# Performance work log

Measured on AMD Instinct MI355X. Metric: run time of the kernel, lower is better.

The kernel has to match this reference:

```python
import jax, jax.numpy as jnp
import numpy as np

D = 256   # input_size
H = 512   # hidden_size
A = 4     # alpha_dim
K = 2 * A * A  # output values per input dim (binary=False -> 2 params)


def _masks():
    # MADE sequential-ordering masks, per DART.create_masks
    in_deg = np.arange(D)
    hid_deg = np.arange(H) % (D - 1)
    out_deg = np.arange(D) - 1  # arange(D) % D - 1
    m0 = (hid_deg[:, None] >= in_deg[None, :]).astype(np.float32)   # [H, D]
    mh = (hid_deg[:, None] >= hid_deg[None, :]).astype(np.float32)  # [H, H]
    ml = (out_deg[:, None] >= hid_deg[None, :]).astype(np.float32)  # [D, H]
    # repeat(1, K).view(-1, H): each output-dim row repeated K consecutive times
    ml = np.repeat(ml, K, axis=0)                                    # [D*K, H]
    return jnp.asarray(m0), jnp.asarray(mh), jnp.asarray(ml)


def setup_inputs() -> dict:
    key = jax.random.key(0)
    ks = jax.random.split(key, 10)
    B = 1024
    x = jax.random.normal(ks[0], (B, D), dtype=jnp.float32)
    def lin(k, out_dim, in_dim):
        s = 1.0 / np.sqrt(in_dim)
        kw, kb = jax.random.split(k)
        W = jax.random.uniform(kw, (out_dim, in_dim), jnp.float32, -s, s)
        b = jax.random.uniform(kb, (out_dim,), jnp.float32, -s, s)
        return W, b
    W0, b0 = lin(ks[1], H, D)
    W1, b1 = lin(ks[2], H, H)
    W2, b2 = lin(ks[3], H, H)
    Wout, bout = lin(ks[4], D * K, H)
    # unnormalized_log_p_alpha initialized to log(1/A)
    ulpa = jnp.full((1, D - 1, 1, A), -np.log(A), dtype=jnp.float32)
    return {"x": x, "W0": W0, "b0": b0, "W1": W1, "b1": b1,
            "W2": W2, "b2": b2, "Wout": Wout, "bout": bout, "ulpa": ulpa}


def reference(x, W0, b0, W1, b1, W2, b2, Wout, bout, ulpa):
    m0, mh, ml = _masks()
    B = x.shape[0]
    # masked MLP (MADE)
    h = jax.nn.relu(x @ (m0 * W0).T + b0)
    h = jax.nn.relu(h @ (mh * W1).T + b1)
    h = jax.nn.relu(h @ (mh * W2).T + b2)
    theta = (h @ (ml * Wout).T + bout).reshape(B, D, 2, A, A)
    mu = theta[:, :, 0]                      # [B, D, A, A]
    std = jnp.exp(theta[:, :, 1]) + 0.01     # [B, D, A, A]
    xe = x[:, :, None, None]
    # Normal log-prob
    log_px = -0.5 * jnp.square((xe - mu) / std) - jnp.log(std) - 0.5 * jnp.log(2.0 * jnp.pi)
    # normalized log p(alpha): [1, D-1, 1, A]
    lpa = jax.nn.log_softmax(ulpa, axis=-1)
    joint = log_px[:, :-1] + lpa             # [B, D-1, A, A]
    first = joint[:, 0, 0:1]                 # [B, 1, A]
    inner = jnp.swapaxes(joint[:, 1:], 0, 1)  # [D-2, B, A, A]
    # HMM-style forward recursion: stable log-domain chain matmul via scan
    def step(carry, m):
        # carry: [B, 1, A]; m: [B, A, A]
        new = jax.nn.logsumexp(carry[:, :, :, None] + m[:, None, :, :], axis=-2)
        return new, None
    carry, _ = jax.lax.scan(step, first, inner)
    last = log_px[:, -1, :, 0:1]             # [B, A, 1]
    log_p = jax.nn.logsumexp(carry[:, :, :, None] + last[:, None, :, :], axis=-2)  # [B,1,1]
    return log_p, theta
```

## Files before the change

### kernel.cpp

```cpp
#include <hip/hip_runtime.h>
#include <math.h>

#define Bsz 1024
#define Dd  256
#define Hh  512
#define NOUT 8192
#define C0f 0.91893853320467274178f

typedef __attribute__((ext_vector_type(8))) short bf8_t;
typedef __attribute__((ext_vector_type(4))) float f4_t;

__device__ inline ushort f2b(float f) {
  union { float f; unsigned u; } c; c.f = f;
  unsigned r = c.u + 0x7fffu + ((c.u >> 16) & 1u);
  return (ushort)(r >> 16);
}

__device__ inline void async16(const void* g, void* l) {
  __builtin_amdgcn_global_load_lds((const __attribute__((address_space(1))) void*)g,
                                   (__attribute__((address_space(3))) void*)l, 16, 0, 0);
}

__device__ inline int mod255(int v) {
  if (v >= 510) return v - 510;
  if (v >= 255) return v - 255;
  return v;
}

__global__ __launch_bounds__(256) void prep(
    const float* __restrict__ x,  const float* __restrict__ W0,
    const float* __restrict__ W1, const float* __restrict__ W2,
    const float* __restrict__ Wout, const float* __restrict__ ulpa,
    ushort* __restrict__ xb, ushort* __restrict__ w0b, ushort* __restrict__ w1b,
    ushort* __restrict__ w2b, ushort* __restrict__ woutb,
    float* __restrict__ lpa)
{
  const int blk = blockIdx.x, tid = threadIdx.x;
  if (blk == 2496) {
    if (tid < Dd - 1) {
      float v0 = ulpa[tid * 4 + 0], v1 = ulpa[tid * 4 + 1];
      float v2 = ulpa[tid * 4 + 2], v3 = ulpa[tid * 4 + 3];
      float m = fmaxf(fmaxf(v0, v1), fmaxf(v2, v3));
      float s = __expf(v0 - m) + __expf(v1 - m) + __expf(v2 - m) + __expf(v3 - m);
      float l = m + __logf(s);
      lpa[tid * 4 + 0] = v0 - l;
      lpa[tid * 4 + 1] = v1 - l;
      lpa[tid * 4 + 2] = v2 - l;
      lpa[tid * 4 + 3] = v3 - l;
    }
    return;
  }
  const float* src; ushort* dst; int lb, mode;
  if (blk < 128)      { src = x;    dst = xb;    lb = blk;       mode = 0; }
  else if (blk < 192) { src = W0;   dst = w0b;   lb = blk - 128; mode = 1; }
  else if (blk < 320) { src = W1;   dst = w1b;   lb = blk - 192; mode = 2; }
  else if (blk < 448) { src = W2;   dst = w2b;   lb = blk - 320; mode = 2; }
  else                { src = Wout; dst = woutb; lb = blk - 448; mode = 3; }

  const int e = lb * 2048 + tid * 8;
  float4 v0 = *(const float4*)(src + e);
  float4 v1 = *(const float4*)(src + e + 4);
  float vv[8] = {v0.x, v0.y, v0.z, v0.w, v1.x, v1.y, v1.z, v1.w};
  ushort u[8];
  if (mode == 0) {
#pragma unroll
    for (int i = 0; i < 8; i++) u[i] = f2b(vv[i]);
  } else if (mode == 1) {
    int n = e >> 8, k0 = e & 255, nd = mod255(n);
#pragma unroll
    for (int i = 0; i < 8; i++) u[i] = (nd >= k0 + i) ? f2b(vv[i]) : (ushort)0;
  } else if (mode == 2) {
    int n = e >> 9, k0 = e & 511, nd = mod255(n);
#pragma unroll
    for (int i = 0; i < 8; i++) u[i] = (nd >= mod255(k0 + i)) ? f2b(vv[i]) : (ushort)0;
  } else {
    int n = e >> 9, k0 = e & 511, nd = (n >> 5) - 1;
#pragma unroll
    for (int i = 0; i < 8; i++) u[i] = (nd >= mod255(k0 + i)) ? f2b(vv[i]) : (ushort)0;
  }
  *(ushort4*)(dst + e)     = *(ushort4*)&u[0];
  *(ushort4*)(dst + e + 4) = *(ushort4*)&u[4];
}

template<int KD>
__global__ __launch_bounds__(256) void gemm_s(
    const ushort* __restrict__ A, const ushort* __restrict__ W,
    const float* __restrict__ bias, ushort* __restrict__ Ch)
{
  __shared__ ushort As[32 * 64];
  __shared__ ushort Bs[32 * 64];
  const int tid = threadIdx.x, lane = tid & 63, wave = tid >> 6;
  const int row0 = blockIdx.y * 32, col0 = blockIdx.x * 32;
  const int wi = wave >> 1, wj = wave & 1;
  const int fm = lane & 15, qq = lane >> 4;
  const int srow = lane >> 3, qslot = lane & 7;

  f4_t acc = (f4_t){0.f, 0.f, 0.f, 0.f};

  for (int kt = 0; kt < KD; kt += 64) {
    {
      int rb = wave * 8;
      int r = rb + srow;
      int q = (qslot - r) & 7;
      async16(A + (size_t)(row0 + r) * KD + kt + q * 8, &As[rb * 64]);
      async16(W + (size_t)(col0 + r) * KD + kt + q * 8, &Bs[rb * 64]);
    }
    __syncthreads();
#pragma unroll
    for (int t = 0; t < 2; t++) {
      int ra = wi * 16 + fm;
      int slota = ((t * 4 + qq) + ra) & 7;
      bf8_t af = *(const bf8_t*)&As[ra * 64 + slota * 8];
      int rb = wj * 16 + fm;
      int slot = ((t * 4 + qq) + rb) & 7;
      bf8_t bf = *(const bf8_t*)&Bs[rb * 64 + slot * 8];
      acc = __builtin_amdgcn_mfma_f32_16x16x32_bf16(af, bf, acc, 0, 0, 0);
    }
    __syncthreads();
  }

  int col = col0 + wj * 16 + fm;
  float bv = bias[col];
  int rbase = row0 + wi * 16 + qq * 4;
#pragma unroll
  for (int r = 0; r < 4; r++) {
    float t = fmaxf(acc[r] + bv, 0.0f);
    Ch[(size_t)(rbase + r) * Hh + col] = f2b(t);
  }
}

__global__ __launch_bounds__(256) void gemm_big(
    const ushort* __restrict__ A, const ushort* __restrict__ W,
    const float* __restrict__ bias, float* __restrict__ Cf)
{
  __shared__ ushort As[128 * 64];
  __shared__ ushort Bs[64 * 64];
  const int tid = threadIdx.x, lane = tid & 63, wave = tid >> 6;
  const int waveM = wave >> 1, waveN = wave & 1;
  const int row0 = blockIdx.y * 128, col0 = blockIdx.x * 64;
  const int dm = 2 * (int)blockIdx.x;
  const int fm = lane & 15, qq = lane >> 4;
  const int srow = lane >> 3, qslot = lane & 7;
  const int Kd = Hh, N = NOUT;

  f4_t acc[4][2];
#pragma unroll
  for (int i = 0; i < 4; i++)
#pragma unroll
    for (int j = 0; j < 2; j++) acc[i][j] = (f4_t){0.f, 0.f, 0.f, 0.f};

  for (int kt = 0; kt < Kd; kt += 64) {
    bool needed = (kt <= dm) || (kt >= 192 && kt <= 255 + dm) || (kt == 448);
    if (!needed) continue;
#pragma unroll
    for (int p = 0; p < 4; p++) {
      int rb = p * 32 + wave * 8;
      int r = rb + srow;
      int q = (qslot - r) & 7;
      async16(A + (size_t)(row0 + r) * Kd + kt + q * 8, &As[rb * 64]);
    }
#pragma unroll
    for (int p = 0; p < 2; p++) {
      int rb = p * 32 + wave * 8;
      int r = rb + srow;
      int q = (qslot - r) & 7;
      async16(W + (size_t)(col0 + r) * Kd + kt + q * 8, &Bs[rb * 64]);
    }
    __syncthreads();
#pragma unroll
    for (int t = 0; t < 2; t++) {
      bf8_t af[4], bf[2];
#pragma unroll
      for (int i = 0; i < 4; i++) {
        int r = waveM * 64 + i * 16 + fm;
        int slot = ((t * 4 + qq) + r) & 7;
        af[i] = *(const bf8_t*)&As[r * 64 + slot * 8];
      }
#pragma unroll
      for (int j = 0; j < 2; j++) {
        int r = waveN * 32 + j * 16 + fm;
        int slot = ((t * 4 + qq) + r) & 7;
        bf[j] = *(const bf8_t*)&Bs[r * 64 + slot * 8];
      }
#pragma unroll
      for (int i = 0; i < 4; i++)
#pragma unroll
        for (int j = 0; j < 2; j++)
          acc[i][j] = __builtin_amdgcn_mfma_f32_16x16x32_bf16(af[i], bf[j], acc[i][j], 0, 0, 0);
    }
    __syncthreads();
  }

#pragma unroll
  for (int j = 0; j < 2; j++) {
    int col = col0 + waveN * 32 + j * 16 + fm;
    float bv = bias[col];
#pragma unroll
    for (int i = 0; i < 4; i++) {
      int rbase = row0 + waveM * 64 + i * 16 + qq * 4;
#pragma unroll
      for (int r = 0; r < 4; r++)
        Cf[(size_t)(rbase + r) * N + col] = acc[i][j][r] + bv;
    }
  }
}

__global__ __launch_bounds__(256) void chain2(
    const float* __restrict__ x, const float* __restrict__ theta,
    const float* __restrict__ lpa, float* __restrict__ logp)
{
  __shared__ float ThS[NOUT];
  __shared__ float XS[Dd];
  __shared__ float Ts[16][16];
  const int b = blockIdx.x;
  const int tid = threadIdx.x, lane = tid & 63, wave = tid >> 6;
  const int seg = tid >> 4, e = tid & 15;
  const int i = e >> 2, jj = e & 3;
  const int base = lane & ~15;
  const float* th = theta + (size_t)b * NOUT;
  const float* xg = x + (size_t)b * Dd;

#pragma unroll
  for (int t = 0; t < 8; t++) {
    int off = (t * 4 + wave) * 256;
    async16(th + off + lane * 4, &ThS[off]);
  }
  if (wave == 0) async16(xg + lane * 4, &XS[0]);
  __syncthreads();

  const int d0 = 1 + seg * 16;
  const int d1 = min(d0 + 16, Dd - 1);

  auto stepm = [&](int d) -> float {
    float mu = ThS[d * 32 + e];
    float ls = ThS[d * 32 + 16 + e];
    float s  = __expf(ls) + 0.01f;
    float z  = (XS[d] - mu) * __builtin_amdgcn_rcpf(s);
    return -0.5f * z * z - __logf(s) - C0f + lpa[d * 4 + jj];
  };

  float T = stepm(d0);
  for (int d = d0 + 1; d < d1; d++) {
    float m_ = stepm(d);
    float v0 = __shfl(T, base + i * 4 + 0) + __shfl(m_, base + 0 * 4 + jj);
    float v1 = __shfl(T, base + i * 4 + 1) + __shfl(m_, base + 1 * 4 + jj);
    float v2 = __shfl(T, base + i * 4 + 2) + __shfl(m_, base + 2 * 4 + jj);
    float v3 = __shfl(T, base + i * 4 + 3) + __shfl(m_, base + 3 * 4 + jj);
    float mx = fmaxf(fmaxf(v0, v1), fmaxf(v2, v3));
    float s  = __expf(v0 - mx) + __expf(v1 - mx) + __expf(v2 - mx) + __expf(v3 - mx);
    T = mx + __logf(s);
  }
  Ts[seg][e] = T;
  __syncthreads();

  if (tid < 4) {
    const int j = tid;
    float mu = ThS[j], ls = ThS[16 + j];
    float s = __expf(ls) + 0.01f;
    float z = (XS[0] - mu) * __builtin_amdgcn_rcpf(s);
    float carry = -0.5f * z * z - __logf(s) - C0f + lpa[j];
#pragma unroll 1
    for (int sg = 0; sg < 16; sg++) {
      float c0 = __shfl(carry, 0);
      float c1 = __shfl(carry, 1);
      float c2 = __shfl(carry, 2);
      float c3 = __shfl(carry, 3);
      float v0 = c0 + Ts[sg][0 * 4 + j];
      float v1 = c1 + Ts[sg][1 * 4 + j];
      float v2 = c2 + Ts[sg][2 * 4 + j];
      float v3 = c3 + Ts[sg][3 * 4 + j];
      float mx = fmaxf(fmaxf(v0, v1), fmaxf(v2, v3));
      float ss = __expf(v0 - mx) + __expf(v1 - mx) + __expf(v2 - mx) + __expf(v3 - mx);
      carry = mx + __logf(ss);
    }
    float mu2 = ThS[255 * 32 + j * 4], ls2 = ThS[255 * 32 + 16 + j * 4];
    float s2 = __expf(ls2) + 0.01f;
    float z2 = (XS[255] - mu2) * __builtin_amdgcn_rcpf(s2);
    float v = carry - 0.5f * z2 * z2 - __logf(s2) - C0f;
    float mx = fmaxf(v, __shfl_xor(v, 1));
    mx = fmaxf(mx, __shfl_xor(mx, 2));
    float ee = __expf(v - mx);
    ee += __shfl_xor(ee, 1);
    ee += __shfl_xor(ee, 2);
    if (j == 0) logp[b] = mx + __logf(ee);
  }
}

extern "C" void kernel_launch(void* const* d_in, const int* in_sizes, int n_in,
                              void* d_out, int out_size, void* d_ws, size_t ws_size,
                              hipStream_t stream)
{
  const float* x    = (const float*)d_in[0];
  const float* W0   = (const float*)d_in[1];
  const float* b0   = (const float*)d_in[2];
  const float* W1   = (const float*)d_in[3];
  const float* b1   = (const float*)d_in[4];
  const float* W2   = (const float*)d_in[5];
  const float* b2   = (const float*)d_in[6];
  const float* Wout = (const float*)d_in[7];
  const float* bout = (const float*)d_in[8];
  const float* ulpa = (const float*)d_in[9];

  float* out   = (float*)d_out;
  float* logp  = out;
  float* theta = out + Bsz;

  ushort* ws    = (ushort*)d_ws;
  ushort* xb    = ws;
  ushort* w0b   = xb + 262144;
  ushort* w1b   = w0b + 131072;
  ushort* w2b   = w1b + 262144;
  ushort* woutb = w2b + 262144;
  ushort* h0    = woutb + 4194304;
  ushort* h1    = h0 + 524288;
  ushort* h2    = h1 + 524288;
  float*  lpa   = (float*)(h2 + 524288);

  prep<<<2497, 256, 0, stream>>>(x, W0, W1, W2, Wout, ulpa,
                                 xb, w0b, w1b, w2b, woutb, lpa);
  gemm_s<Dd><<<dim3(16, 32), 256, 0, stream>>>(xb, w0b, b0, h0);
  gemm_s<Hh><<<dim3(16, 32), 256, 0, stream>>>(h0, w1b, b1, h1);
  gemm_s<Hh><<<dim3(16, 32), 256, 0, stream>>>(h1, w2b, b2, h2);
  gemm_big<<<dim3(NOUT / 64, Bsz / 128), 256, 0, stream>>>(h2, woutb, bout, theta);
  chain2<<<Bsz, 256, 0, stream>>>(x, theta, lpa, logp);
}
```

Measured before the change: 138.6 us.

## Fuse three hidden-layer GEMMs into one persistent kernel with grid barriers

Replaces the three separate small hidden-layer GEMM launches with a single 512-block kernel that computes each layer tile and then waits on a software grid-wide barrier (atomic counter reset in prep) before the next layer. The aim is to remove two kernel launch gaps and their tail effects. It relies on all 512 blocks being co-resident; otherwise it deadlocks. The atomic spin barrier also adds its own latency.

Result: slower. 258.8 us (+86.7%).

```diff
diff --git a/kernel.cpp b/kernel.cpp
--- a/kernel.cpp
+++ b/kernel.cpp
@@ -33,10 +33,11 @@
     const float* __restrict__ Wout, const float* __restrict__ ulpa,
     ushort* __restrict__ xb, ushort* __restrict__ w0b, ushort* __restrict__ w1b,
     ushort* __restrict__ w2b, ushort* __restrict__ woutb,
-    float* __restrict__ lpa)
+    float* __restrict__ lpa, unsigned* __restrict__ bar)
 {
   const int blk = blockIdx.x, tid = threadIdx.x;
   if (blk == 2496) {
+    if (tid < 16) bar[tid] = 0u;
     if (tid < Dd - 1) {
       float v0 = ulpa[tid * 4 + 0], v1 = ulpa[tid * 4 + 1];
       float v2 = ulpa[tid * 4 + 2], v3 = ulpa[tid * 4 + 3];
@@ -82,15 +83,26 @@
   *(ushort4*)(dst + e + 4) = *(ushort4*)&u[4];
 }
 
+__device__ inline void gridbar(unsigned* bar, unsigned target) {
+  __syncthreads();
+  if (threadIdx.x == 0) {
+    __threadfence();
+    __hip_atomic_fetch_add(bar, 1u, __ATOMIC_ACQ_REL, __HIP_MEMORY_SCOPE_AGENT);
+    while (__hip_atomic_load(bar, __ATOMIC_RELAXED, __HIP_MEMORY_SCOPE_AGENT) < target)
+      __builtin_amdgcn_s_sleep(4);
+    (void)__hip_atomic_load(bar, __ATOMIC_ACQUIRE, __HIP_MEMORY_SCOPE_AGENT);
+  }
+  __syncthreads();
+  __threadfence();
+}
+
 template<int KD>
-__global__ __launch_bounds__(256) void gemm_s(
+__device__ __forceinline__ void layer_tile(
     const ushort* __restrict__ A, const ushort* __restrict__ W,
-    const float* __restrict__ bias, ushort* __restrict__ Ch)
-{
-  __shared__ ushort As[32 * 64];
-  __shared__ ushort Bs[32 * 64];
+    const float* __restrict__ bias, ushort* __restrict__ Ch,
+    int row0, int col0, ushort* As, ushort* Bs)
+{
   const int tid = threadIdx.x, lane = tid & 63, wave = tid >> 6;
-  const int row0 = blockIdx.y * 32, col0 = blockIdx.x * 32;
   const int wi = wave >> 1, wj = wave & 1;
   const int fm = lane & 15, qq = lane >> 4;
   const int srow = lane >> 3, qslot = lane & 7;
@@ -127,6 +139,26 @@
     float t = fmaxf(acc[r] + bv, 0.0f);
     Ch[(size_t)(rbase + r) * Hh + col] = f2b(t);
   }
+}
+
+__global__ __launch_bounds__(256) void mlp3(
+    const ushort* __restrict__ xb,
+    const ushort* __restrict__ w0b, const float* __restrict__ b0,
+    const ushort* __restrict__ w1b, const float* __restrict__ b1,
+    const ushort* __restrict__ w2b, const float* __restrict__ b2,
+    ushort* __restrict__ h0, ushort* __restrict__ h1, ushort* __restrict__ h2,
+    unsigned* __restrict__ bar)
+{
+  __shared__ ushort As[32 * 64];
+  __shared__ ushort Bs[32 * 64];
+  const int row0 = (blockIdx.x >> 4) * 32;
+  const int col0 = (blockIdx.x & 15) * 32;
+
+  layer_tile<Dd>(xb, w0b, b0, h0, row0, col0, As, Bs);
+  gridbar(bar, 512);
+  layer_tile<Hh>(h0, w1b, b1, h1, row0, col0, As, Bs);
+  gridbar(bar, 1024);
+  layer_tile<Hh>(h1, w2b, b2, h2, row0, col0, As, Bs);
 }
 
 __global__ __launch_bounds__(256) void gemm_big(
@@ -315,12 +347,11 @@
   ushort* h1    = h0 + 524288;
   ushort* h2    = h1 + 524288;
   float*  lpa   = (float*)(h2 + 524288);
+  unsigned* bar = (unsigned*)(lpa + 1024);
 
   prep<<<2497, 256, 0, stream>>>(x, W0, W1, W2, Wout, ulpa,
-                                 xb, w0b, w1b, w2b, woutb, lpa);
-  gemm_s<Dd><<<dim3(16, 32), 256, 0, stream>>>(xb, w0b, b0, h0);
-  gemm_s<Hh><<<dim3(16, 32), 256, 0, stream>>>(h0, w1b, b1, h1);
-  gemm_s<Hh><<<dim3(16, 32), 256, 0, stream>>>(h1, w2b, b2, h2);
+                                 xb, w0b, w1b, w2b, woutb, lpa, bar);
+  mlp3<<<512, 256, 0, stream>>>(xb, w0b, b0, w1b, b1, w2b, b2, h0, h1, h2, bar);
   gemm_big<<<dim3(NOUT / 64, Bsz / 128), 256, 0, stream>>>(h2, woutb, bout, theta);
   chain2<<<Bsz, 256, 0, stream>>>(x, theta, lpa, logp);
 }
```
